# Optimization experiments

Measured on AMD Instinct MI355X. Metric: run time of the kernel, lower is better.

The kernel has to match this reference:

```python
import jax, jax.numpy as jnp
import numpy as np

B, H, W, C = 2, 128, 128, 96
L = H * W
NUM_HEADS = 6
D_STATE = 16
DT_RANK = 6  # ceil(96/16)
D_CONV = 4
MLP_HIDDEN = 4 * C


def _layernorm(x, g, b, eps=1e-5):
    m = x.mean(-1, keepdims=True)
    v = x.var(-1, keepdims=True)
    return (x - m) * jax.lax.rsqrt(v + eps) * g + b


def _dwconv2d(x, w, b):
    # x: [B,C,H,W], w: [C,1,3,3] depthwise, padding=1 (torch 'same' for k=3)
    y = jax.lax.conv_general_dilated(x, w, (1, 1), [(1, 1), (1, 1)],
                                     dimension_numbers=('NCHW', 'OIHW', 'NCHW'),
                                     feature_group_count=x.shape[1])
    return y + b[None, :, None, None]


def _dwconv1d(x, w):
    # x: [B,C,L], w: [C,1,4]; torch padding='same' for even k=4 pads (1,2); bias is None (conv_bias//2 == 0)
    return jax.lax.conv_general_dilated(x, w, (1,), [(1, 2)],
                                        dimension_numbers=('NCH', 'OIH', 'NCH'),
                                        feature_group_count=x.shape[1])


def _rope(x):
    # x: [b, H, W, c]; 2D axial rotary embedding, k_max = c//4 per axis
    b, h, w, c = x.shape
    k_max = c // 4
    theta = 1.0 / (10000.0 ** (jnp.arange(k_max, dtype=jnp.float32) / k_max))
    ang_h = jnp.broadcast_to(jnp.arange(h, dtype=jnp.float32)[:, None, None] * theta, (h, w, k_max))
    ang_w = jnp.broadcast_to(jnp.arange(w, dtype=jnp.float32)[None, :, None] * theta, (h, w, k_max))
    angles = jnp.concatenate([ang_h, ang_w], -1)  # [h,w,c//2]
    cos, sin = jnp.cos(angles), jnp.sin(angles)
    xr, xi = x[..., 0::2], x[..., 1::2]  # consecutive pairs -> complex
    out_r = xr * cos - xi * sin
    out_i = xr * sin + xi * cos
    return jnp.stack([out_r, out_i], -1).reshape(x.shape)


def _linear_attention(x, qk_w, qk_b, lepe_w, lepe_b):
    # x: [b, n, c]
    b, n, c = x.shape
    hd = c // NUM_HEADS
    qk = x @ qk_w + qk_b  # [b,n,2c]
    q = jax.nn.elu(qk[..., :c]) + 1.0
    k = jax.nn.elu(qk[..., c:]) + 1.0
    v = x
    q_r = _rope(q.reshape(b, H, W, c)).reshape(b, n, NUM_HEADS, hd).transpose(0, 2, 1, 3)
    k_r = _rope(k.reshape(b, H, W, c)).reshape(b, n, NUM_HEADS, hd).transpose(0, 2, 1, 3)
    qh = q.reshape(b, n, NUM_HEADS, hd).transpose(0, 2, 1, 3)
    kh = k.reshape(b, n, NUM_HEADS, hd).transpose(0, 2, 1, 3)
    vh = v.reshape(b, n, NUM_HEADS, hd).transpose(0, 2, 1, 3)
    kmean = kh.mean(axis=2, keepdims=True)  # [b,h,1,hd]
    zden = 1.0 / (jnp.einsum('bhnd,bhmd->bhnm', qh, kmean) + 1e-6)  # [b,h,n,1]
    scale = n ** (-0.5)
    kv = jnp.einsum('bhnd,bhne->bhde', k_r * scale, vh * scale)  # [b,h,hd,hd]
    out = jnp.einsum('bhnd,bhde->bhne', q_r, kv) * zden
    out = out.transpose(0, 2, 1, 3).reshape(b, n, c)
    v2d = v.reshape(b, H, W, c).transpose(0, 3, 1, 2)
    lepe = _dwconv2d(v2d, lepe_w, lepe_b).transpose(0, 2, 3, 1).reshape(b, n, c)
    return out + lepe


def _selective_scan(u, delta, A, Bm, Cm, Dv):
    # u, delta: [b,d,l]; A: [d,n]; Bm, Cm: [b,n,l]; Dv: [d]
    dA = jnp.exp(jnp.einsum('bdl,dn->lbdn', delta, A))
    dBu = jnp.einsum('bdl,bnl,bdl->lbdn', delta, Bm, u)
    Ct = jnp.moveaxis(Cm, -1, 0)  # [l,b,n]

    def step(hcar, inp):
        dA_t, dBu_t, C_t = inp
        hcar = dA_t * hcar + dBu_t  # [b,d,n]
        y_t = jnp.einsum('bdn,bn->bd', hcar, C_t)
        return hcar, y_t

    h0 = jnp.zeros(dA.shape[1:], dtype=u.dtype)
    _, ys = jax.lax.scan(step, h0, (dA, dBu, Ct))  # ys: [l,b,d]
    y = jnp.moveaxis(ys, 0, -1)  # [b,d,l]
    return y + Dv[None, :, None] * u


def setup_inputs() -> dict:
    key = jax.random.key(0)
    ks = iter(jax.random.split(key, 40))

    def rn(shape, s=0.02):
        return jax.random.normal(next(ks), shape, jnp.float32) * s

    dt = jnp.exp(jax.random.uniform(next(ks), (C,), jnp.float32)
                 * (np.log(0.1) - np.log(0.001)) + np.log(0.001))
    dt_proj_b = dt + jnp.log(-jnp.expm1(-dt))
    return {
        'hidden_states': jax.random.normal(next(ks), (B, L, C), jnp.float32),
        'norm_in_g': jnp.ones((C,), jnp.float32),
        'norm_in_b': jnp.zeros((C,), jnp.float32),
        'in_proj_w': rn((C, 3 * C)),
        'dw_w': rn((C, 1, 3, 3)),
        'dw_b': rn((C,)),
        'qk_w': rn((C, 2 * C)),
        'qk_b': rn((2 * C,)),
        'lepe_w': rn((C, 1, 3, 3)),
        'lepe_b': rn((C,)),
        'conv_x_w': rn((C, 1, D_CONV)),
        'conv_z_w': rn((C, 1, D_CONV)),
        'x_proj_w': rn((C, DT_RANK + 2 * D_STATE)),
        'dt_proj_w': rn((DT_RANK, C), DT_RANK ** -0.5),
        'dt_proj_b': dt_proj_b,
        'A_log': jnp.log(jnp.broadcast_to(jnp.arange(1, D_STATE + 1, dtype=jnp.float32), (C, D_STATE)) + 0.0),
        'D': jnp.ones((C,), jnp.float32),
        'out_proj_w': rn((2 * C, C)),
        'proj_out_w': rn((C, C)),
        'proj_out_b': rn((C,)),
        'out_w': rn((2 * C, C)),
        'out_b': rn((C,)),
        'norm_mlp_g': jnp.ones((C,), jnp.float32),
        'norm_mlp_b': jnp.zeros((C,), jnp.float32),
        'fc1_w': rn((C, MLP_HIDDEN)),
        'fc1_b': rn((MLP_HIDDEN,)),
        'fc2_w': rn((MLP_HIDDEN, C)),
        'fc2_b': rn((C,)),
    }


def reference(hidden_states, norm_in_g, norm_in_b, in_proj_w, dw_w, dw_b, qk_w, qk_b,
              lepe_w, lepe_b, conv_x_w, conv_z_w, x_proj_w, dt_proj_w, dt_proj_b,
              A_log, D, out_proj_w, proj_out_w, proj_out_b, out_w, out_b,
              norm_mlp_g, norm_mlp_b, fc1_w, fc1_b, fc2_w, fc2_b):
    b, l, c = hidden_states.shape
    shortcut = hidden_states
    hs = _layernorm(hidden_states, norm_in_g, norm_in_b)
    xzw = jnp.transpose(hs @ in_proj_w, (0, 2, 1))  # [b,3c,l]
    x, z, w_ = jnp.split(xzw, 3, axis=1)  # each [b,c,l]
    # linear-attention branch
    lin_x = jax.nn.silu(_dwconv2d(w_.reshape(b, c, H, W), dw_w, dw_b))
    lin_x = jnp.transpose(lin_x, (0, 2, 3, 1)).reshape(b, l, c)
    lin_x = _linear_attention(lin_x, qk_w, qk_b, lepe_w, lepe_b)
    # selective-scan branch
    A = -jnp.exp(A_log)
    x = jax.nn.silu(_dwconv1d(x, conv_x_w))
    z = jax.nn.silu(_dwconv1d(z, conv_z_w))
    x_dbl = jnp.einsum('bdl,de->ble', x, x_proj_w)
    dt = x_dbl[..., :DT_RANK]
    Bm = jnp.transpose(x_dbl[..., DT_RANK:DT_RANK + D_STATE], (0, 2, 1))
    Cm = jnp.transpose(x_dbl[..., DT_RANK + D_STATE:], (0, 2, 1))
    delta = jax.nn.softplus(jnp.einsum('blr,rd->bdl', dt, dt_proj_w) + dt_proj_b[None, :, None])
    y = _selective_scan(x, delta, A, Bm, Cm, D)
    y = jnp.concatenate([y, z], axis=1)  # [b,2c,l]
    out1 = jnp.transpose(y, (0, 2, 1)) @ out_proj_w  # [b,l,c]
    z_t = jnp.transpose(z, (0, 2, 1))
    out2 = (lin_x * z_t) @ proj_out_w + proj_out_b
    out = jnp.concatenate([out1, out2], -1) @ out_w + out_b
    out = shortcut + out
    h2 = _layernorm(out, norm_mlp_g, norm_mlp_b)
    h2 = jax.nn.gelu(h2 @ fc1_w + fc1_b, approximate=False)
    return out + (h2 @ fc2_w + fc2_b)
```

## Files before the change

### kernel.cpp

```cpp
#include <hip/hip_runtime.h>
#include <hip/hip_bf16.h>
#include <math.h>

#define B_ 2
#define H_ 128
#define W_ 128
#define C_ 96
#define L_ (H_*W_)
#define BL_ (B_*L_)
#define NH_ 6
#define NPROJ_ 38
#define MLPH_ 384
#define NCH_ 512
#define CHL_ (L_/NCH_)
#define NG_ 32

typedef __attribute__((ext_vector_type(8))) short bf16x8;
typedef __attribute__((ext_vector_type(4))) float f32x4;

#define MFMA16(a,b,c) __builtin_amdgcn_mfma_f32_16x16x32_bf16(a,b,c,0,0,0)

#define WOFF1 0
#define WOFF2 54
#define WOFF3 90
#define WOFF4 126
#define WOFF5 144
#define WOFF6 180
#define WOFF7 252
#define WOFF8 324
#define WFRAGS 333

__device__ __forceinline__ float siluf(float x){ return x / (1.f + __expf(-x)); }
__device__ __forceinline__ unsigned short f2bf(float x){
    __hip_bfloat16 h = __float2bfloat16(x);
    return *reinterpret_cast<unsigned short*>(&h);
}
__device__ __forceinline__ unsigned pack2(float a, float b){
    return (unsigned)f2bf(a) | ((unsigned)f2bf(b) << 16);
}
__device__ __forceinline__ float bf2f(unsigned short u){
    return __uint_as_float((unsigned)u << 16);
}
__device__ __forceinline__ float gelu_fast(float x){
    float u_ = 0.7978845608f*x*(1.f + 0.044715f*x*x);
    float au = fabsf(u_);
    float e = __expf(-2.f*au);
    float th = (1.f - e)/(1.f + e);
    th = copysignf(th, u_);
    return 0.5f*x*(1.f + th);
}

__global__ __launch_bounds__(64) void k_setup(const float* __restrict__ w1,
    const float* __restrict__ w2, const float* __restrict__ w3,
    const float* __restrict__ w4, const float* __restrict__ w5,
    const float* __restrict__ w6, const float* __restrict__ w7,
    const float* __restrict__ dww, const float* __restrict__ lw,
    const float* __restrict__ xpw, const float* __restrict__ cxw,
    const float* __restrict__ czw,
    unsigned short* __restrict__ dst, float2* __restrict__ ctab,
    float* __restrict__ wt9, float* __restrict__ lw9, float* __restrict__ kvacc,
    float* __restrict__ wxT, float* __restrict__ wzT)
{
    int m = blockIdx.y;
    int l = threadIdx.x;
    if (m < 7){
        const float* srcs[7] = {w1,w2,w3,w4,w5,w6,w7};
        const int Ks[7]   = {96,96,192,96,192,96,384};
        const int Ns[7]   = {288,192,96,96,96,384,96};
        const int offs[7] = {WOFF1,WOFF2,WOFF3,WOFF4,WOFF5,WOFF6,WOFF7};
        int f = blockIdx.x;
        int nnt = Ns[m] >> 4, nkf = Ks[m] >> 5;
        if (f >= nnt*nkf) return;
        int kf = f / nnt, nt = f - kf*nnt;
        const float* s = srcs[m];
        unsigned short* d = dst + ((size_t)(offs[m] + f)*64 + l)*8;
        int krow = kf*32 + (l>>4)*8;
        int col  = nt*16 + (l&15);
        #pragma unroll
        for (int j=0;j<8;j++) d[j] = f2bf(s[(size_t)(krow+j)*Ns[m] + col]);
    } else {
        int x = blockIdx.x;
        if (x == 0){
            for (int i=l; i<128*24; i+=64){
                int pos = i/24, p = i%24;
                float th = powf(10000.f, -(float)p/24.f);
                float sn, cs; sincosf((float)pos*th, &sn, &cs);
                ctab[i] = make_float2(cs, sn);
            }
        } else if (x == 1){
            for (int i=l; i<3264; i+=64) kvacc[i] = 0.f;
        } else if (x == 2){
            for (int i=l; i<864; i+=64){
                int c = i/9, tap = i%9;
                wt9[tap*96 + c] = dww[i];
                lw9[tap*96 + c] = lw[i];
            }
        } else if (x == 3){
            for (int f=0; f<9; f++){
                int kf=f/3, nt=f%3;
                unsigned short* d = dst + ((size_t)(WOFF8 + f)*64 + l)*8;
                int krow = kf*32 + (l>>4)*8;
                int col  = nt*16 + (l&15);
                #pragma unroll
                for (int j=0;j<8;j++){
                    float v = (col < NPROJ_) ? xpw[(size_t)(krow+j)*NPROJ_ + col] : 0.f;
                    d[j] = f2bf(v);
                }
            }
        } else if (x == 4){
            for (int i=l; i<384; i+=64){
                int j = i/96, c = i%96;
                wxT[i] = cxw[c*4 + j];
                wzT[i] = czw[c*4 + j];
            }
        }
    }
}

__global__ __launch_bounds__(256) void k_ln_inproj_m(const float* __restrict__ hs,
    const float* __restrict__ gg, const float* __restrict__ bb,
    const unsigned short* __restrict__ wbf,
    float* __restrict__ xx, float* __restrict__ zz, float* __restrict__ ww)
{
    __shared__ unsigned short A[64*128];
    int t = threadIdx.x;
    size_t row0 = (size_t)blockIdx.x * 64;
    {
        int r = t >> 2, q = t & 3;
        const float* src = hs + (row0 + r)*C_ + q*24;
        float v[24];
        float s=0.f, s2=0.f;
        #pragma unroll
        for (int i=0;i<24;i++){ float x=src[i]; v[i]=x; s+=x; s2+=x*x; }
        s += __shfl_xor(s,1); s2 += __shfl_xor(s2,1);
        s += __shfl_xor(s,2); s2 += __shfl_xor(s2,2);
        float mn = s*(1.f/C_);
        float rs = rsqrtf(s2*(1.f/C_) - mn*mn + 1e-5f);
        int base = r*128, sw = (r&7)<<3;
        #pragma unroll
        for (int i=0;i<24;i+=2){
            int c = q*24 + i;
            float a0 = (v[i]  -mn)*rs*gg[c]   + bb[c];
            float a1 = (v[i+1]-mn)*rs*gg[c+1] + bb[c+1];
            *(unsigned*)&A[base + (c ^ sw)] = pack2(a0,a1);
        }
    }
    __syncthreads();
    int w = t>>6, l = t&63, lr = l&15, lh = l>>4;
    int arow = w*16 + lr;
    int abase = arow*128, asw = (arow&7)<<3;
    bf16x8 af[3];
    #pragma unroll
    for (int kf=0;kf<3;kf++)
        af[kf] = *(const bf16x8*)&A[abase + ((kf*32 + lh*8) ^ asw)];
    #pragma unroll 2
    for (int nt=0; nt<18; nt++){
        f32x4 acc = {0.f,0.f,0.f,0.f};
        #pragma unroll
        for (int kf=0;kf<3;kf++){
            bf16x8 bf_ = *(const bf16x8*)(wbf + ((size_t)((WOFF1 + kf*18 + nt)*64 + l))*8);
            acc = MFMA16(af[kf], bf_, acc);
        }
        float* base_;
        if (nt < 6) base_ = xx; else if (nt < 12) base_ = zz; else base_ = ww;
        int col = (nt%6)*16 + lr;
        float* dst = base_ + (row0 + w*16 + lh*4)*C_ + col;
        #pragma unroll
        for (int j=0;j<4;j++) dst[(size_t)j*C_] = acc[j];
    }
}

__global__ __launch_bounds__(256) void k_dwconv2d(const float* __restrict__ wwb,
    const float* __restrict__ wt9, const float* __restrict__ dwb,
    float* __restrict__ out)
{
    int gid = blockIdx.x*256 + threadIdx.x;
    int row = gid/24, c4 = gid%24; int c = c4*4;
    int b = row >> 14;
    int ll = row & (L_-1);
    int h = ll >> 7, wq = ll & 127;
    float4 acc = {0.f,0.f,0.f,0.f};
    #pragma unroll
    for (int kh=0; kh<3; kh++){
        int hh = h + kh - 1;
        if ((unsigned)hh < 128u){
            int base_row = (b<<14) + (hh<<7);
            #pragma unroll
            for (int kw=0; kw<3; kw++){
                int wp = wq + kw - 1;
                if ((unsigned)wp < 128u){
                    float4 v = *(const float4*)&wwb[(size_t)(base_row + wp)*C_ + c];
                    float4 wt = *(const float4*)&wt9[(kh*3+kw)*96 + c];
                    acc.x += v.x*wt.x; acc.y += v.y*wt.y;
                    acc.z += v.z*wt.z; acc.w += v.w*wt.w;
                }
            }
        }
    }
    float4 bv = *(const float4*)&dwb[c];
    float4 o;
    o.x = siluf(acc.x+bv.x); o.y = siluf(acc.y+bv.y);
    o.z = siluf(acc.z+bv.z); o.w = siluf(acc.w+bv.w);
    *(float4*)&out[(size_t)row*C_ + c] = o;
}

__global__ __launch_bounds__(256) void k_conv1d_xdbl(const float* __restrict__ xxb,
    const float* __restrict__ zzb, const float* __restrict__ wxT,
    const float* __restrict__ wzT, const unsigned short* __restrict__ wbf,
    const float* __restrict__ dtw, const float* __restrict__ dtb,
    float* __restrict__ xs, float* __restrict__ zs,
    float* __restrict__ delta, float* __restrict__ BC)
{
    __shared__ unsigned short A[64*128];
    __shared__ float XD[64][8];
    __shared__ float dtws[6][96];
    int t = threadIdx.x;
    size_t row0 = (size_t)blockIdx.x * 64;
    int b = (int)(row0 >> 14);
    int l0 = (int)(row0 & 16383);
    for (int i=t; i<576; i+=256) dtws[i/96][i%96] = dtw[i];
    for (int p=t; p<64*24; p+=256){
        int r = p/24, cq = p - r*24, c = cq*4;
        int l = l0 + r;
        float ax0=0.f,ax1=0.f,ax2=0.f,ax3=0.f;
        float az0=0.f,az1=0.f,az2=0.f,az3=0.f;
        #pragma unroll
        for (int j=0;j<4;j++){
            int lq = l - 1 + j;
            if ((unsigned)lq < (unsigned)L_){
                size_t off = ((size_t)(b<<14) + lq)*C_ + c;
                float4 xv = *(const float4*)&xxb[off];
                float4 zv = *(const float4*)&zzb[off];
                float4 wx4 = *(const float4*)&wxT[j*96 + c];
                float4 wz4 = *(const float4*)&wzT[j*96 + c];
                ax0 += xv.x*wx4.x; ax1 += xv.y*wx4.y; ax2 += xv.z*wx4.z; ax3 += xv.w*wx4.w;
                az0 += zv.x*wz4.x; az1 += zv.y*wz4.y; az2 += zv.z*wz4.z; az3 += zv.w*wz4.w;
            }
        }
        ax0=siluf(ax0); ax1=siluf(ax1); ax2=siluf(ax2); ax3=siluf(ax3);
        az0=siluf(az0); az1=siluf(az1); az2=siluf(az2); az3=siluf(az3);
        float4 xo={ax0,ax1,ax2,ax3}, zo={az0,az1,az2,az3};
        *(float4*)&xs[(row0+r)*C_ + c] = xo;
        *(float4*)&zs[(row0+r)*C_ + c] = zo;
        int sw = (r&7)<<3;
        uint2 pk = { pack2(ax0,ax1), pack2(ax2,ax3) };
        *(uint2*)&A[r*128 + (c ^ sw)] = pk;
    }
    __syncthreads();
    int w=t>>6, l=t&63, lr=l&15, lh=l>>4;
    int arow = w*16+lr, asw=(arow&7)<<3;
    bf16x8 af[3];
    #pragma unroll
    for (int kf=0;kf<3;kf++)
        af[kf] = *(const bf16x8*)&A[arow*128 + ((kf*32 + lh*8) ^ asw)];
    #pragma unroll
    for (int nt=0; nt<3; nt++){
        f32x4 acc={0.f,0.f,0.f,0.f};
        #pragma unroll
        for (int kf=0;kf<3;kf++){
            bf16x8 bfr=*(const bf16x8*)(wbf + ((size_t)((WOFF8 + kf*3 + nt)*64 + l))*8);
            acc = MFMA16(af[kf], bfr, acc);
        }
        int col = nt*16 + lr;
        #pragma unroll
        for (int j=0;j<4;j++){
            int row = w*16 + lh*4 + j;
            if (col < 6) XD[row][col] = acc[j];
            else if (col < NPROJ_) BC[(row0+row)*32 + (col-6)] = acc[j];
        }
    }
    __syncthreads();
    {
        int r = t>>2, q = t&3;
        float xd0=XD[r][0], xd1=XD[r][1], xd2=XD[r][2];
        float xd3=XD[r][3], xd4=XD[r][4], xd5=XD[r][5];
        #pragma unroll
        for (int g=0; g<6; g++){
            int c = q*24 + g*4;
            float4 acc = *(const float4*)&dtb[c];
            float4 w0 = *(const float4*)&dtws[0][c];
            float4 w1 = *(const float4*)&dtws[1][c];
            float4 w2 = *(const float4*)&dtws[2][c];
            float4 w3 = *(const float4*)&dtws[3][c];
            float4 w4 = *(const float4*)&dtws[4][c];
            float4 w5 = *(const float4*)&dtws[5][c];
            acc.x += xd0*w0.x + xd1*w1.x + xd2*w2.x + xd3*w3.x + xd4*w4.x + xd5*w5.x;
            acc.y += xd0*w0.y + xd1*w1.y + xd2*w2.y + xd3*w3.y + xd4*w4.y + xd5*w5.y;
            acc.z += xd0*w0.z + xd1*w1.z + xd2*w2.z + xd3*w3.z + xd4*w4.z + xd5*w5.z;
            acc.w += xd0*w0.w + xd1*w1.w + xd2*w2.w + xd3*w3.w + xd4*w4.w + xd5*w5.w;
            float4 dl;
            dl.x = (acc.x>20.f)? acc.x : __logf(1.f+__expf(acc.x));
            dl.y = (acc.y>20.f)? acc.y : __logf(1.f+__expf(acc.y));
            dl.z = (acc.z>20.f)? acc.z : __logf(1.f+__expf(acc.z));
            dl.w = (acc.w>20.f)? acc.w : __logf(1.f+__expf(acc.w));
            *(float4*)&delta[(row0+r)*C_ + c] = dl;
        }
    }
}

__global__ __launch_bounds__(256) void k_qk_kv(const float* __restrict__ lin,
    const unsigned short* __restrict__ wbf, const float* __restrict__ qkb,
    const float2* __restrict__ ctab, float* __restrict__ qo,
    float* __restrict__ kvacc)
{
    __shared__ unsigned short A[64*128];
    __shared__ float KR[64*105];
    __shared__ float kmsum[96];
    int t = threadIdx.x;
    size_t row0 = (size_t)blockIdx.x * 64;
    int b = (int)(row0 >> 14);
    int l0 = (int)(row0 & 16383);
    for (int p = t; p < 64*48; p += 256){
        int r = p/48, c = (p - r*48)*2;
        float2 xy = *(const float2*)&lin[(row0 + r)*C_ + c];
        *(unsigned*)&A[r*128 + (c ^ ((r&7)<<3))] = pack2(xy.x, xy.y);
    }
    if (t < 96) kmsum[t] = 0.f;
    __syncthreads();
    int w=t>>6, l=t&63, lr=l&15, lh=l>>4;
    int arow = w*16+lr; int asw=(arow&7)<<3;
    bf16x8 af[3];
    #pragma unroll
    for (int kf=0;kf<3;kf++)
        af[kf] = *(const bf16x8*)&A[arow*128 + ((kf*32 + lh*8) ^ asw)];
    #pragma unroll 2
    for (int nt=0; nt<12; nt++){
        f32x4 acc={0.f,0.f,0.f,0.f};
        #pragma unroll
        for (int kf=0;kf<3;kf++){
            bf16x8 bfr=*(const bf16x8*)(wbf + ((size_t)((WOFF2 + kf*12 + nt)*64 + l))*8);
            acc = MFMA16(af[kf], bfr, acc);
        }
        int colg = nt*16 + lr;
        float bias = qkb[colg];
        float vv[4];
        #pragma unroll
        for (int j=0;j<4;j++){
            float v = acc[j] + bias;
            vv[j] = (v>0.f)? v+1.f : __expf(v);
        }
        if (nt < 6){
            float* dp = qo + (row0 + w*16 + lh*4)*C_ + colg;
            #pragma unroll
            for (int j=0;j<4;j++) dp[(size_t)j*C_] = vv[j];
        } else {
            int ck = colg - 96;
            atomicAdd(&kmsum[ck], vv[0]+vv[1]+vv[2]+vv[3]);
            float pv[4];
            #pragma unroll
            for (int j=0;j<4;j++) pv[j] = __shfl_xor(vv[j], 1);
            int p = ck >> 1;
            #pragma unroll
            for (int j=0;j<4;j++){
                int rl = l0 + w*16 + lh*4 + j;
                int hp = rl>>7, wp = rl&127;
                float2 cssn = (p<24)? ctab[hp*24+p] : ctab[wp*24+(p-24)];
                float kr = (ck&1)? (pv[j]*cssn.y + vv[j]*cssn.x)
                                 : (vv[j]*cssn.x - pv[j]*cssn.y);
                KR[(w*16+lh*4+j)*105 + ck] = kr;
            }
        }
    }
    __syncthreads();
    for (int h = w; h < 6; h += 4){
        f32x4 acc = {0.f,0.f,0.f,0.f};
        #pragma unroll
        for (int kk=0; kk<2; kk++){
            union { bf16x8 v; unsigned short u[8]; } afu, bfu;
            #pragma unroll
            for (int j=0;j<8;j++){
                int rr = kk*32 + lh*8 + j;
                afu.u[j] = f2bf(KR[rr*105 + h*16 + lr]);
                bfu.u[j] = A[rr*128 + ((h*16+lr) ^ ((rr&7)<<3))];
            }
            acc = MFMA16(afu.v, bfu.v, acc);
        }
        #pragma unroll
        for (int i=0;i<4;i++)
            atomicAdd(&kvacc[b*1536 + h*256 + (lh*4+i)*16 + lr], acc[i]);
    }
    if (t < 96) atomicAdd(&kvacc[3072 + b*96 + t], kmsum[t]);
}

__global__ __launch_bounds__(384) void k_attnout(const float* __restrict__ qbuf,
    const float* __restrict__ vbuf, const float* __restrict__ kvacc,
    const float2* __restrict__ ctab, const float* __restrict__ lw9,
    const float* __restrict__ lb, float* __restrict__ aout)
{
    __shared__ float kvs[1536];
    __shared__ float kms[96];
    int t = threadIdx.x;
    size_t row0 = (size_t)blockIdx.x * 16;
    int b = (int)(row0 >> 14);
    const float invL = 1.f/16384.f;
    for (int i=t; i<1536; i+=384) kvs[i] = kvacc[b*1536+i]*invL;
    if (t < 96) kms[t] = kvacc[3072+b*96+t]*invL;
    __syncthreads();
    int r = t/24, c4 = t%24;
    int c = c4*4;
    int lrow = (int)(row0 & 16383) + r;
    int hp = lrow>>7, wp = lrow&127;
    size_t row = row0 + r;
    float4 q4 = *(const float4*)&qbuf[row*C_ + c];
    int p0 = c>>1, p1 = p0+1;
    float2 cs0 = (p0<24)? ctab[hp*24+p0] : ctab[wp*24+(p0-24)];
    float2 cs1 = (p1<24)? ctab[hp*24+p1] : ctab[wp*24+(p1-24)];
    float4 qr;
    qr.x = q4.x*cs0.x - q4.y*cs0.y;
    qr.y = q4.x*cs0.y + q4.y*cs0.x;
    qr.z = q4.z*cs1.x - q4.w*cs1.y;
    qr.w = q4.z*cs1.y + q4.w*cs1.x;
    int h = c4>>2, j = c4&3;
    int dbase = j*4;
    float zp = q4.x*kms[h*16+dbase]   + q4.y*kms[h*16+dbase+1]
             + q4.z*kms[h*16+dbase+2] + q4.w*kms[h*16+dbase+3];
    zp += __shfl_xor(zp,1);
    zp += __shfl_xor(zp,2);
    float zd = 1.f/(zp + 1e-6f);
    float4 o = {0.f,0.f,0.f,0.f};
    #pragma unroll
    for (int g=0; g<4; g++){
        float4 qg;
        if (g==0) qg = qr;
        else {
            qg.x=__shfl_xor(qr.x,g); qg.y=__shfl_xor(qr.y,g);
            qg.z=__shfl_xor(qr.z,g); qg.w=__shfl_xor(qr.w,g);
        }
        int db = ((j^g)<<2);
        const float* kp = &kvs[h*256 + db*16 + j*4];
        #pragma unroll
        for (int i=0;i<4;i++){
            float qi = (i==0)?qg.x:(i==1)?qg.y:(i==2)?qg.z:qg.w;
            float4 kv4 = *(const float4*)&kp[i*16];
            o.x += qi*kv4.x; o.y += qi*kv4.y;
            o.z += qi*kv4.z; o.w += qi*kv4.w;
        }
    }
    float4 acc = *(const float4*)&lb[c];
    #pragma unroll
    for (int kh=0; kh<3; kh++){
        int hh = hp + kh - 1;
        if ((unsigned)hh < 128u){
            int base_row = (b<<14) + (hh<<7);
            #pragma unroll
            for (int kw=0; kw<3; kw++){
                int wq = wp + kw - 1;
                if ((unsigned)wq < 128u){
                    float4 v = *(const float4*)&vbuf[(size_t)(base_row + wq)*C_ + c];
                    float4 wt = *(const float4*)&lw9[(kh*3+kw)*96 + c];
                    acc.x += v.x*wt.x; acc.y += v.y*wt.y;
                    acc.z += v.z*wt.z; acc.w += v.w*wt.w;
                }
            }
        }
    }
    float4 res;
    res.x = o.x*zd + acc.x; res.y = o.y*zd + acc.y;
    res.z = o.z*zd + acc.z; res.w = o.w*zd + acc.w;
    *(float4*)&aout[row*C_ + c] = res;
}

__global__ __launch_bounds__(384) void k_scan1(const float* __restrict__ delta,
    const float* __restrict__ xs, const float* __restrict__ BC,
    const float* __restrict__ A_log, float* __restrict__ Ap, float* __restrict__ Be)
{
    int t = threadIdx.x; int nq = t&3, c = t>>2;
    int blk = blockIdx.x; int b = blk>>9, ch = blk&(NCH_-1);
    float4 a4 = *(const float4*)&A_log[c*16 + nq*4];
    float a0=-__expf(a4.x), a1=-__expf(a4.y), a2=-__expf(a4.z), a3=-__expf(a4.w);
    float ap0=1.f,ap1=1.f,ap2=1.f,ap3=1.f;
    float be0=0.f,be1=0.f,be2=0.f,be3=0.f;
    size_t base = ((size_t)b<<14) + ch*CHL_;
    for (int i=0;i<CHL_;i++){
        size_t row = base + i;
        float dl = delta[row*C_+c];
        float u  = xs[row*C_+c];
        float du = dl*u;
        float4 bc = *(const float4*)&BC[row*32 + nq*4];
        float e0=__expf(dl*a0), e1=__expf(dl*a1), e2=__expf(dl*a2), e3=__expf(dl*a3);
        ap0*=e0; be0=be0*e0+du*bc.x;
        ap1*=e1; be1=be1*e1+du*bc.y;
        ap2*=e2; be2=be2*e2+du*bc.z;
        ap3*=e3; be3=be3*e3+du*bc.w;
    }
    size_t o = (size_t)blk*1536 + c*16 + nq*4;
    float4 apv={ap0,ap1,ap2,ap3}, bev={be0,be1,be2,be3};
    *(float4*)&Ap[o] = apv;
    *(float4*)&Be[o] = bev;
}

__global__ __launch_bounds__(384) void k_scan2a(const float* __restrict__ Ap,
    const float* __restrict__ Be, float* __restrict__ GA, float* __restrict__ GB)
{
    int t = threadIdx.x; int blk = blockIdx.x;
    int b = blk>>5, g = blk&(NG_-1);
    int idx = (t>>2)*16 + (t&3)*4;
    float4 A = {1.f,1.f,1.f,1.f}, Bv = {0.f,0.f,0.f,0.f};
    for (int j=0;j<16;j++){
        size_t o = ((size_t)(b*NCH_ + g*16 + j))*1536 + idx;
        float4 a = *(const float4*)&Ap[o];
        float4 bb = *(const float4*)&Be[o];
        Bv.x=a.x*Bv.x+bb.x; Bv.y=a.y*Bv.y+bb.y; Bv.z=a.z*Bv.z+bb.z; Bv.w=a.w*Bv.w+bb.w;
        A.x*=a.x; A.y*=a.y; A.z*=a.z; A.w*=a.w;
    }
    size_t o = (size_t)blk*1536 + idx;
    *(float4*)&GA[o] = A;
    *(float4*)&GB[o] = Bv;
}

__global__ __launch_bounds__(256) void k_scan2b(const float* __restrict__ GA,
    const float* __restrict__ GB, float* __restrict__ Gin)
{
    int t = blockIdx.x*256 + threadIdx.x;
    int b = t/1536, m = t%1536;
    float h = 0.f;
    for (int g=0; g<NG_; g++){
        size_t o = ((size_t)(b*NG_+g))*1536 + m;
        Gin[o] = h;
        h = GA[o]*h + GB[o];
    }
}

__global__ __launch_bounds__(384) void k_scan2c(const float* __restrict__ Ap,
    const float* __restrict__ Be, const float* __restrict__ Gin,
    float* __restrict__ Hin)
{
    int t = threadIdx.x; int blk = blockIdx.x;
    int b = blk>>5, g = blk&(NG_-1);
    int idx = (t>>2)*16 + (t&3)*4;
    float4 h = *(const float4*)&Gin[(size_t)blk*1536 + idx];
    for (int j=0;j<16;j++){
        size_t o = ((size_t)(b*NCH_ + g*16 + j))*1536 + idx;
        *(float4*)&Hin[o] = h;
        float4 a = *(const float4*)&Ap[o];
        float4 bb = *(const float4*)&Be[o];
        h.x=a.x*h.x+bb.x; h.y=a.y*h.y+bb.y; h.z=a.z*h.z+bb.z; h.w=a.w*h.w+bb.w;
    }
}

__global__ __launch_bounds__(384) void k_scan3(const float* __restrict__ delta,
    const float* __restrict__ xs, const float* __restrict__ BC,
    const float* __restrict__ A_log, const float* __restrict__ Dv,
    const float* __restrict__ Hin, float* __restrict__ y)
{
    int t = threadIdx.x; int nq = t&3, c = t>>2;
    int blk = blockIdx.x; int b = blk>>9, ch = blk&(NCH_-1);
    float4 a4 = *(const float4*)&A_log[c*16 + nq*4];
    float a0=-__expf(a4.x), a1=-__expf(a4.y), a2=-__expf(a4.z), a3=-__expf(a4.w);
    float4 h = *(const float4*)&Hin[(size_t)blk*1536 + c*16 + nq*4];
    float Dc = Dv[c];
    size_t base = ((size_t)b<<14) + ch*CHL_;
    for (int i=0;i<CHL_;i++){
        size_t row = base + i;
        float dl = delta[row*C_+c];
        float u  = xs[row*C_+c];
        float du = dl*u;
        float4 bcB = *(const float4*)&BC[row*32 + nq*4];
        float4 bcC = *(const float4*)&BC[row*32 + 16 + nq*4];
        float e0=__expf(dl*a0), e1=__expf(dl*a1), e2=__expf(dl*a2), e3=__expf(dl*a3);
        h.x=h.x*e0+du*bcB.x; h.y=h.y*e1+du*bcB.y;
        h.z=h.z*e2+du*bcB.z; h.w=h.w*e3+du*bcB.w;
        float yv = h.x*bcC.x + h.y*bcC.y + h.z*bcC.z + h.w*bcC.w;
        yv += __shfl_xor(yv,1);
        yv += __shfl_xor(yv,2);
        if (nq == 0) y[row*C_+c] = yv + Dc*u;
    }
}

__global__ __launch_bounds__(512) void k_combine_mlp(const float* __restrict__ y,
    const float* __restrict__ zs, const float* __restrict__ aout,
    const unsigned short* __restrict__ wbf, const float* __restrict__ pob,
    const float* __restrict__ outb, const float* __restrict__ hs,
    const float* __restrict__ gg, const float* __restrict__ bb,
    const float* __restrict__ f1b, const float* __restrict__ f2b,
    float* __restrict__ outr)
{
    __shared__ __attribute__((aligned(16))) char POOL[65536];
    __shared__ float LNS[64][2], LNS2[64][2];
    unsigned short* Y  = (unsigned short*)POOL;
    unsigned short* AZ = (unsigned short*)(POOL + 24576);
    unsigned short* C2 = (unsigned short*)(POOL + 40960);
    unsigned short* AT = (unsigned short*)POOL;
    unsigned short* HID= (unsigned short*)(POOL + 16384);
    int t=threadIdx.x;
    size_t row0=(size_t)blockIdx.x*64;
    for (int p=t;p<64*48;p+=512){
        int r=p/48, c=(p-r*48)*2;
        size_t g=(row0+r)*C_+c;
        float2 yv=*(const float2*)&y[g];
        float2 zv=*(const float2*)&zs[g];
        float2 av=*(const float2*)&aout[g];
        int sw=(r&7)<<3;
        *(unsigned*)&Y[r*192 + (c^sw)] = pack2(yv.x,yv.y);
        *(unsigned*)&Y[r*192 + ((96+c)^sw)] = pack2(zv.x,zv.y);
        *(unsigned*)&AZ[r*128 + (c^sw)] = pack2(av.x*zv.x, av.y*zv.y);
    }
    __syncthreads();
    int w=t>>6, l=t&63, lr=l&15, lh=l>>4;
    int rt=w>>1, hf=w&1;
    int arow=rt*16+lr; int asw=(arow&7)<<3;
    bf16x8 af1[6], af2[3];
    #pragma unroll
    for (int kf=0;kf<6;kf++) af1[kf]=*(const bf16x8*)&Y[arow*192 + ((kf*32+lh*8)^asw)];
    #pragma unroll
    for (int kf=0;kf<3;kf++) af2[kf]=*(const bf16x8*)&AZ[arow*128 + ((kf*32+lh*8)^asw)];
    #pragma unroll
    for (int q=0;q<3;q++){
        int nt = hf*3 + q;
        f32x4 a1={0.f,0.f,0.f,0.f}, a2={0.f,0.f,0.f,0.f};
        #pragma unroll
        for (int kf=0;kf<6;kf++){
            bf16x8 b=*(const bf16x8*)(wbf+((size_t)((WOFF3+kf*6+nt)*64+l))*8);
            a1=MFMA16(af1[kf],b,a1);
        }
        #pragma unroll
        for (int kf=0;kf<3;kf++){
            bf16x8 b=*(const bf16x8*)(wbf+((size_t)((WOFF4+kf*6+nt)*64+l))*8);
            a2=MFMA16(af2[kf],b,a2);
        }
        int col=nt*16+lr;
        float pb=pob[col];
        #pragma unroll
        for (int j=0;j<4;j++){
            int row=rt*16+lh*4+j;
            int sw2=(row&7)<<3;
            C2[row*192 + (col^sw2)] = f2bf(a1[j]);
            C2[row*192 + ((96+col)^sw2)] = f2bf(a2[j]+pb);
        }
    }
    __syncthreads();
    bf16x8 af3[6];
    #pragma unroll
    for (int kf=0;kf<6;kf++) af3[kf]=*(const bf16x8*)&C2[arow*192 + ((kf*32+lh*8)^asw)];
    float outv[3][4];
    #pragma unroll
    for (int q=0;q<3;q++){
        int nt = hf*3 + q;
        f32x4 acc={0.f,0.f,0.f,0.f};
        #pragma unroll
        for (int kf=0;kf<6;kf++){
            bf16x8 b=*(const bf16x8*)(wbf+((size_t)((WOFF5+kf*6+nt)*64+l))*8);
            acc=MFMA16(af3[kf],b,acc);
        }
        int col=nt*16+lr;
        float ob=outb[col];
        #pragma unroll
        for (int j=0;j<4;j++){
            size_t row=row0+rt*16+lh*4+j;
            outv[q][j] = acc[j] + ob + hs[row*C_+col];
        }
    }
    float s_[4], s2_[4];
    #pragma unroll
    for (int j=0;j<4;j++){
        float s=0.f, s2=0.f;
        #pragma unroll
        for (int q=0;q<3;q++){ float v=outv[q][j]; s+=v; s2+=v*v; }
        s_[j]=s; s2_[j]=s2;
    }
    #pragma unroll
    for (int m=1;m<16;m<<=1){
        #pragma unroll
        for (int j=0;j<4;j++){
            s_[j]  += __shfl_xor(s_[j],  m);
            s2_[j] += __shfl_xor(s2_[j], m);
        }
    }
    if (lr==0){
        #pragma unroll
        for (int j=0;j<4;j++){
            int row = rt*16+lh*4+j;
            LNS[row][hf]  = s_[j];
            LNS2[row][hf] = s2_[j];
        }
    }
    __syncthreads();
    #pragma unroll
    for (int j=0;j<4;j++){
        int row = rt*16+lh*4+j;
        float s  = LNS[row][0]  + LNS[row][1];
        float s2 = LNS2[row][0] + LNS2[row][1];
        float mn = s*(1.f/C_);
        float rs = rsqrtf(s2*(1.f/C_) - mn*mn + 1e-5f);
        int sw2 = (row&7)<<3;
        #pragma unroll
        for (int q=0;q<3;q++){
            int col = (hf*3+q)*16+lr;
            AT[row*128 + (col^sw2)] = f2bf((outv[q][j]-mn)*rs*gg[col]+bb[col]);
        }
    }
    __syncthreads();
    {
        bf16x8 af[3];
        #pragma unroll
        for(int kf=0;kf<3;kf++) af[kf]=*(const bf16x8*)&AT[arow*128+((kf*32+lh*8)^asw)];
        #pragma unroll 2
        for(int q=0;q<12;q++){
            int nt = hf*12 + q;
            f32x4 acc={0.f,0.f,0.f,0.f};
            #pragma unroll
            for(int kf=0;kf<3;kf++){
                bf16x8 b=*(const bf16x8*)(wbf+((size_t)((WOFF6+kf*24+nt)*64+l))*8);
                acc=MFMA16(af[kf],b,acc);
            }
            int col=nt*16+lr;
            float bias=f1b[col];
            #pragma unroll
            for(int j=0;j<4;j++){
                int row=rt*16+lh*4+j;
                HID[row*384 + (col^((row&7)<<3))] = f2bf(gelu_fast(acc[j]+bias));
            }
        }
    }
    __syncthreads();
    {
        bf16x8 afh[12];
        #pragma unroll
        for(int kf=0;kf<12;kf++) afh[kf]=*(const bf16x8*)&HID[arow*384+((kf*32+lh*8)^asw)];
        #pragma unroll
        for(int q=0;q<3;q++){
            int nt = hf*3 + q;
            f32x4 acc={0.f,0.f,0.f,0.f};
            #pragma unroll
            for(int kf=0;kf<12;kf++){
                bf16x8 b=*(const bf16x8*)(wbf+((size_t)((WOFF7+kf*6+nt)*64+l))*8);
                acc=MFMA16(afh[kf],b,acc);
            }
            int col=nt*16+lr;
            float bias=f2b[col];
            #pragma unroll
            for(int j=0;j<4;j++){
                size_t row=row0+rt*16+lh*4+j;
                outr[row*C_+col] = outv[q][j] + acc[j] + bias;
            }
        }
    }
}

extern "C" void kernel_launch(void* const* d_in, const int* in_sizes, int n_in,
                              void* d_out, int out_size, void* d_ws, size_t ws_size,
                              hipStream_t stream)
{
    const float* hs        = (const float*)d_in[0];
    const float* norm_in_g = (const float*)d_in[1];
    const float* norm_in_b = (const float*)d_in[2];
    const float* in_proj_w = (const float*)d_in[3];
    const float* dw_w      = (const float*)d_in[4];
    const float* dw_b      = (const float*)d_in[5];
    const float* qk_w      = (const float*)d_in[6];
    const float* qk_b      = (const float*)d_in[7];
    const float* lepe_w    = (const float*)d_in[8];
    const float* lepe_b    = (const float*)d_in[9];
    const float* conv_x_w  = (const float*)d_in[10];
    const float* conv_z_w  = (const float*)d_in[11];
    const float* x_proj_w  = (const float*)d_in[12];
    const float* dt_proj_w = (const float*)d_in[13];
    const float* dt_proj_b = (const float*)d_in[14];
    const float* A_log     = (const float*)d_in[15];
    const float* Dv        = (const float*)d_in[16];
    const float* out_proj_w= (const float*)d_in[17];
    const float* proj_out_w= (const float*)d_in[18];
    const float* proj_out_b= (const float*)d_in[19];
    const float* out_w     = (const float*)d_in[20];
    const float* out_b     = (const float*)d_in[21];
    const float* norm_mlp_g= (const float*)d_in[22];
    const float* norm_mlp_b= (const float*)d_in[23];
    const float* fc1_w     = (const float*)d_in[24];
    const float* fc1_b     = (const float*)d_in[25];
    const float* fc2_w     = (const float*)d_in[26];
    const float* fc2_b     = (const float*)d_in[27];

    float* ws = (float*)d_ws;
    size_t o = 0;
    float* xx    = ws + o; o += (size_t)BL_*C_;
    float* zz    = ws + o; o += (size_t)BL_*C_;
    float* wwb   = ws + o; o += (size_t)BL_*C_;
    float* lin_x = ws + o; o += (size_t)BL_*C_;
    float* xs    = ws + o; o += (size_t)BL_*C_;
    float* zs    = ws + o; o += (size_t)BL_*C_;
    float* delta = ws + o; o += (size_t)BL_*C_;
    float* BC    = ws + o; o += (size_t)BL_*32;
    float* Ap    = ws + o; o += (size_t)B_*NCH_*1536;
    float* Be    = ws + o; o += (size_t)B_*NCH_*1536;
    float* Hin   = ws + o; o += (size_t)B_*NCH_*1536;
    float* GA    = ws + o; o += (size_t)B_*NG_*1536;
    float* GB    = ws + o; o += (size_t)B_*NG_*1536;
    float* Gin   = ws + o; o += (size_t)B_*NG_*1536;
    float* kvacc = ws + o; o += 3264;
    float2* ctab = (float2*)(ws + o); o += 6144;
    float* wt9   = ws + o; o += 864;
    float* lw9   = ws + o; o += 864;
    float* wxT   = ws + o; o += 384;
    float* wzT   = ws + o; o += 384;
    unsigned short* wbf = (unsigned short*)(ws + o);

    float* qbuf = xx;
    float* ybuf = zz;
    float* aout = wwb;
    float* outr = (float*)d_out;

    k_setup<<<dim3(72,8), 64, 0, stream>>>(in_proj_w, qk_w, out_proj_w, proj_out_w,
                                           out_w, fc1_w, fc2_w, dw_w, lepe_w,
                                           x_proj_w, conv_x_w, conv_z_w,
                                           wbf, ctab, wt9, lw9, kvacc, wxT, wzT);
    k_ln_inproj_m<<<BL_/64, 256, 0, stream>>>(hs, norm_in_g, norm_in_b, wbf, xx, zz, wwb);
    k_dwconv2d<<<(BL_*24)/256, 256, 0, stream>>>(wwb, wt9, dw_b, lin_x);
    k_conv1d_xdbl<<<BL_/64, 256, 0, stream>>>(xx, zz, wxT, wzT, wbf,
                                              dt_proj_w, dt_proj_b, xs, zs, delta, BC);
    k_qk_kv<<<BL_/64, 256, 0, stream>>>(lin_x, wbf, qk_b, ctab, qbuf, kvacc);
    k_attnout<<<BL_/16, 384, 0, stream>>>(qbuf, lin_x, kvacc, ctab, lw9, lepe_b, aout);
    k_scan1<<<B_*NCH_, 384, 0, stream>>>(delta, xs, BC, A_log, Ap, Be);
    k_scan2a<<<B_*NG_, 384, 0, stream>>>(Ap, Be, GA, GB);
    k_scan2b<<<12, 256, 0, stream>>>(GA, GB, Gin);
    k_scan2c<<<B_*NG_, 384, 0, stream>>>(Ap, Be, Gin, Hin);
    k_scan3<<<B_*NCH_, 384, 0, stream>>>(delta, xs, BC, A_log, Dv, Hin, ybuf);
    k_combine_mlp<<<BL_/64, 512, 0, stream>>>(ybuf, zs, aout, wbf, proj_out_b,
                                              out_b, hs, norm_mlp_g, norm_mlp_b,
                                              fc1_b, fc2_b, outr);
}
```

Measured before the change: 203.2 us.

## Store intermediate activations as bf16 and fuse z gating into attention output

Intermediate buffers (in-projection x/z/w outputs, dwconv output, q, z-silu, scan y, gated attention output) are now written and read as bf16 instead of fp32. This roughly halves global memory traffic between the chain of kernels. The multiplication of the attention output by z moves into k_attnout, so k_combine_mlp loads MFMA A-fragments straight from global memory without the LDS staging pass. The cost is extra rounding of intermediates to bf16, which may hurt accuracy.

```diff
diff --git a/kernel.cpp b/kernel.cpp
--- a/kernel.cpp
+++ b/kernel.cpp
@@ -17,6 +17,7 @@
 
 typedef __attribute__((ext_vector_type(8))) short bf16x8;
 typedef __attribute__((ext_vector_type(4))) float f32x4;
+typedef __attribute__((ext_vector_type(4))) unsigned short us4v;
 
 #define MFMA16(a,b,c) __builtin_amdgcn_mfma_f32_16x16x32_bf16(a,b,c,0,0,0)
 
@@ -120,7 +121,8 @@
 __global__ __launch_bounds__(256) void k_ln_inproj_m(const float* __restrict__ hs,
     const float* __restrict__ gg, const float* __restrict__ bb,
     const unsigned short* __restrict__ wbf,
-    float* __restrict__ xx, float* __restrict__ zz, float* __restrict__ ww)
+    unsigned short* __restrict__ xx, unsigned short* __restrict__ zz,
+    unsigned short* __restrict__ ww)
 {
     __shared__ unsigned short A[64*128];
     int t = threadIdx.x;
@@ -161,25 +163,25 @@
             bf16x8 bf_ = *(const bf16x8*)(wbf + ((size_t)((WOFF1 + kf*18 + nt)*64 + l))*8);
             acc = MFMA16(af[kf], bf_, acc);
         }
-        float* base_;
+        unsigned short* base_;
         if (nt < 6) base_ = xx; else if (nt < 12) base_ = zz; else base_ = ww;
         int col = (nt%6)*16 + lr;
-        float* dst = base_ + (row0 + w*16 + lh*4)*C_ + col;
-        #pragma unroll
-        for (int j=0;j<4;j++) dst[(size_t)j*C_] = acc[j];
-    }
-}
-
-__global__ __launch_bounds__(256) void k_dwconv2d(const float* __restrict__ wwb,
+        unsigned short* dst = base_ + (row0 + w*16 + lh*4)*C_ + col;
+        #pragma unroll
+        for (int j=0;j<4;j++) dst[(size_t)j*C_] = f2bf(acc[j]);
+    }
+}
+
+__global__ __launch_bounds__(256) void k_dwconv2d(const unsigned short* __restrict__ wwb,
     const float* __restrict__ wt9, const float* __restrict__ dwb,
-    float* __restrict__ out)
+    unsigned short* __restrict__ out)
 {
     int gid = blockIdx.x*256 + threadIdx.x;
     int row = gid/24, c4 = gid%24; int c = c4*4;
     int b = row >> 14;
     int ll = row & (L_-1);
     int h = ll >> 7, wq = ll & 127;
-    float4 acc = {0.f,0.f,0.f,0.f};
+    float a0=0.f,a1=0.f,a2=0.f,a3=0.f;
     #pragma unroll
     for (int kh=0; kh<3; kh++){
         int hh = h + kh - 1;
@@ -189,26 +191,26 @@
             for (int kw=0; kw<3; kw++){
                 int wp = wq + kw - 1;
                 if ((unsigned)wp < 128u){
-                    float4 v = *(const float4*)&wwb[(size_t)(base_row + wp)*C_ + c];
+                    us4v v = *(const us4v*)&wwb[(size_t)(base_row + wp)*C_ + c];
                     float4 wt = *(const float4*)&wt9[(kh*3+kw)*96 + c];
-                    acc.x += v.x*wt.x; acc.y += v.y*wt.y;
-                    acc.z += v.z*wt.z; acc.w += v.w*wt.w;
+                    a0 += bf2f(v[0])*wt.x; a1 += bf2f(v[1])*wt.y;
+                    a2 += bf2f(v[2])*wt.z; a3 += bf2f(v[3])*wt.w;
                 }
             }
         }
     }
     float4 bv = *(const float4*)&dwb[c];
-    float4 o;
-    o.x = siluf(acc.x+bv.x); o.y = siluf(acc.y+bv.y);
-    o.z = siluf(acc.z+bv.z); o.w = siluf(acc.w+bv.w);
-    *(float4*)&out[(size_t)row*C_ + c] = o;
-}
-
-__global__ __launch_bounds__(256) void k_conv1d_xdbl(const float* __restrict__ xxb,
-    const float* __restrict__ zzb, const float* __restrict__ wxT,
+    us4v o;
+    o[0]=f2bf(siluf(a0+bv.x)); o[1]=f2bf(siluf(a1+bv.y));
+    o[2]=f2bf(siluf(a2+bv.z)); o[3]=f2bf(siluf(a3+bv.w));
+    *(us4v*)&out[(size_t)row*C_ + c] = o;
+}
+
+__global__ __launch_bounds__(256) void k_conv1d_xdbl(const unsigned short* __restrict__ xxb,
+    const unsigned short* __restrict__ zzb, const float* __restrict__ wxT,
     const float* __restrict__ wzT, const unsigned short* __restrict__ wbf,
     const float* __restrict__ dtw, const float* __restrict__ dtb,
-    float* __restrict__ xs, float* __restrict__ zs,
+    float* __restrict__ xs, unsigned short* __restrict__ zb,
     float* __restrict__ delta, float* __restrict__ BC)
 {
     __shared__ unsigned short A[64*128];
@@ -229,19 +231,22 @@
             int lq = l - 1 + j;
             if ((unsigned)lq < (unsigned)L_){
                 size_t off = ((size_t)(b<<14) + lq)*C_ + c;
-                float4 xv = *(const float4*)&xxb[off];
-                float4 zv = *(const float4*)&zzb[off];
+                us4v xv = *(const us4v*)&xxb[off];
+                us4v zv = *(const us4v*)&zzb[off];
                 float4 wx4 = *(const float4*)&wxT[j*96 + c];
                 float4 wz4 = *(const float4*)&wzT[j*96 + c];
-                ax0 += xv.x*wx4.x; ax1 += xv.y*wx4.y; ax2 += xv.z*wx4.z; ax3 += xv.w*wx4.w;
-                az0 += zv.x*wz4.x; az1 += zv.y*wz4.y; az2 += zv.z*wz4.z; az3 += zv.w*wz4.w;
+                ax0 += bf2f(xv[0])*wx4.x; ax1 += bf2f(xv[1])*wx4.y;
+                ax2 += bf2f(xv[2])*wx4.z; ax3 += bf2f(xv[3])*wx4.w;
+                az0 += bf2f(zv[0])*wz4.x; az1 += bf2f(zv[1])*wz4.y;
+                az2 += bf2f(zv[2])*wz4.z; az3 += bf2f(zv[3])*wz4.w;
             }
         }
         ax0=siluf(ax0); ax1=siluf(ax1); ax2=siluf(ax2); ax3=siluf(ax3);
         az0=siluf(az0); az1=siluf(az1); az2=siluf(az2); az3=siluf(az3);
-        float4 xo={ax0,ax1,ax2,ax3}, zo={az0,az1,az2,az3};
+        float4 xo={ax0,ax1,ax2,ax3};
         *(float4*)&xs[(row0+r)*C_ + c] = xo;
-        *(float4*)&zs[(row0+r)*C_ + c] = zo;
+        us4v zo; zo[0]=f2bf(az0); zo[1]=f2bf(az1); zo[2]=f2bf(az2); zo[3]=f2bf(az3);
+        *(us4v*)&zb[(row0+r)*C_ + c] = zo;
         int sw = (r&7)<<3;
         uint2 pk = { pack2(ax0,ax1), pack2(ax2,ax3) };
         *(uint2*)&A[r*128 + (c ^ sw)] = pk;
@@ -298,9 +303,9 @@
     }
 }
 
-__global__ __launch_bounds__(256) void k_qk_kv(const float* __restrict__ lin,
+__global__ __launch_bounds__(256) void k_qk_kv(const unsigned short* __restrict__ lin,
     const unsigned short* __restrict__ wbf, const float* __restrict__ qkb,
-    const float2* __restrict__ ctab, float* __restrict__ qo,
+    const float2* __restrict__ ctab, unsigned short* __restrict__ qo,
     float* __restrict__ kvacc)
 {
     __shared__ unsigned short A[64*128];
@@ -310,10 +315,10 @@
     size_t row0 = (size_t)blockIdx.x * 64;
     int b = (int)(row0 >> 14);
     int l0 = (int)(row0 & 16383);
-    for (int p = t; p < 64*48; p += 256){
-        int r = p/48, c = (p - r*48)*2;
-        float2 xy = *(const float2*)&lin[(row0 + r)*C_ + c];
-        *(unsigned*)&A[r*128 + (c ^ ((r&7)<<3))] = pack2(xy.x, xy.y);
+    for (int p = t; p < 64*12; p += 256){
+        int r = p/12, c = (p - r*12)*8;
+        int sw = (r&7)<<3;
+        *(uint4*)&A[r*128 + (c ^ sw)] = *(const uint4*)&lin[(row0+r)*C_ + c];
     }
     if (t < 96) kmsum[t] = 0.f;
     __syncthreads();
@@ -340,9 +345,9 @@
             vv[j] = (v>0.f)? v+1.f : __expf(v);
         }
         if (nt < 6){
-            float* dp = qo + (row0 + w*16 + lh*4)*C_ + colg;
-            #pragma unroll
-            for (int j=0;j<4;j++) dp[(size_t)j*C_] = vv[j];
+            unsigned short* dp = qo + (row0 + w*16 + lh*4)*C_ + colg;
+            #pragma unroll
+            for (int j=0;j<4;j++) dp[(size_t)j*C_] = f2bf(vv[j]);
         } else {
             int ck = colg - 96;
             atomicAdd(&kmsum[ck], vv[0]+vv[1]+vv[2]+vv[3]);
@@ -382,10 +387,11 @@
     if (t < 96) atomicAdd(&kvacc[3072 + b*96 + t], kmsum[t]);
 }
 
-__global__ __launch_bounds__(384) void k_attnout(const float* __restrict__ qbuf,
-    const float* __restrict__ vbuf, const float* __restrict__ kvacc,
-    const float2* __restrict__ ctab, const float* __restrict__ lw9,
-    const float* __restrict__ lb, float* __restrict__ aout)
+__global__ __launch_bounds__(384) void k_attnout(const unsigned short* __restrict__ qb,
+    const unsigned short* __restrict__ vb, const unsigned short* __restrict__ zb,
+    const float* __restrict__ kvacc, const float2* __restrict__ ctab,
+    const float* __restrict__ lw9, const float* __restrict__ lb,
+    unsigned short* __restrict__ azb)
 {
     __shared__ float kvs[1536];
     __shared__ float kms[96];
@@ -401,19 +407,20 @@
     int lrow = (int)(row0 & 16383) + r;
     int hp = lrow>>7, wp = lrow&127;
     size_t row = row0 + r;
-    float4 q4 = *(const float4*)&qbuf[row*C_ + c];
+    us4v qu = *(const us4v*)&qb[row*C_ + c];
+    float q0=bf2f(qu[0]), q1=bf2f(qu[1]), q2=bf2f(qu[2]), q3=bf2f(qu[3]);
     int p0 = c>>1, p1 = p0+1;
     float2 cs0 = (p0<24)? ctab[hp*24+p0] : ctab[wp*24+(p0-24)];
     float2 cs1 = (p1<24)? ctab[hp*24+p1] : ctab[wp*24+(p1-24)];
     float4 qr;
-    qr.x = q4.x*cs0.x - q4.y*cs0.y;
-    qr.y = q4.x*cs0.y + q4.y*cs0.x;
-    qr.z = q4.z*cs1.x - q4.w*cs1.y;
-    qr.w = q4.z*cs1.y + q4.w*cs1.x;
+    qr.x = q0*cs0.x - q1*cs0.y;
+    qr.y = q0*cs0.y + q1*cs0.x;
+    qr.z = q2*cs1.x - q3*cs1.y;
+    qr.w = q2*cs1.y + q3*cs1.x;
     int h = c4>>2, j = c4&3;
     int dbase = j*4;
-    float zp = q4.x*kms[h*16+dbase]   + q4.y*kms[h*16+dbase+1]
-             + q4.z*kms[h*16+dbase+2] + q4.w*kms[h*16+dbase+3];
+    float zp = q0*kms[h*16+dbase]   + q1*kms[h*16+dbase+1]
+             + q2*kms[h*16+dbase+2] + q3*kms[h*16+dbase+3];
     zp += __shfl_xor(zp,1);
     zp += __shfl_xor(zp,2);
     float zd = 1.f/(zp + 1e-6f);
@@ -446,18 +453,21 @@
             for (int kw=0; kw<3; kw++){
                 int wq = wp + kw - 1;
                 if ((unsigned)wq < 128u){
-                    float4 v = *(const float4*)&vbuf[(size_t)(base_row + wq)*C_ + c];
+                    us4v v = *(const us4v*)&vb[(size_t)(base_row + wq)*C_ + c];
                     float4 wt = *(const float4*)&lw9[(kh*3+kw)*96 + c];
-                    acc.x += v.x*wt.x; acc.y += v.y*wt.y;
-                    acc.z += v.z*wt.z; acc.w += v.w*wt.w;
+                    acc.x += bf2f(v[0])*wt.x; acc.y += bf2f(v[1])*wt.y;
+                    acc.z += bf2f(v[2])*wt.z; acc.w += bf2f(v[3])*wt.w;
                 }
             }
         }
     }
-    float4 res;
-    res.x = o.x*zd + acc.x; res.y = o.y*zd + acc.y;
-    res.z = o.z*zd + acc.z; res.w = o.w*zd + acc.w;
-    *(float4*)&aout[row*C_ + c] = res;
+    us4v zu = *(const us4v*)&zb[row*C_ + c];
+    us4v res;
+    res[0] = f2bf((o.x*zd + acc.x)*bf2f(zu[0]));
+    res[1] = f2bf((o.y*zd + acc.y)*bf2f(zu[1]));
+    res[2] = f2bf((o.z*zd + acc.z)*bf2f(zu[2]));
+    res[3] = f2bf((o.w*zd + acc.w)*bf2f(zu[3]));
+    *(us4v*)&azb[row*C_ + c] = res;
 }
 
 __global__ __launch_bounds__(384) void k_scan1(const float* __restrict__ delta,
@@ -541,7 +551,7 @@
 __global__ __launch_bounds__(384) void k_scan3(const float* __restrict__ delta,
     const float* __restrict__ xs, const float* __restrict__ BC,
     const float* __restrict__ A_log, const float* __restrict__ Dv,
-    const float* __restrict__ Hin, float* __restrict__ y)
+    const float* __restrict__ Hin, unsigned short* __restrict__ y)
 {
     int t = threadIdx.x; int nq = t&3, c = t>>2;
     int blk = blockIdx.x; int b = blk>>9, ch = blk&(NCH_-1);
@@ -563,12 +573,12 @@
         float yv = h.x*bcC.x + h.y*bcC.y + h.z*bcC.z + h.w*bcC.w;
         yv += __shfl_xor(yv,1);
         yv += __shfl_xor(yv,2);
-        if (nq == 0) y[row*C_+c] = yv + Dc*u;
-    }
-}
-
-__global__ __launch_bounds__(512) void k_combine_mlp(const float* __restrict__ y,
-    const float* __restrict__ zs, const float* __restrict__ aout,
+        if (nq == 0) y[row*C_+c] = f2bf(yv + Dc*u);
+    }
+}
+
+__global__ __launch_bounds__(512) void k_combine_mlp(const unsigned short* __restrict__ yb,
+    const unsigned short* __restrict__ zb, const unsigned short* __restrict__ azb,
     const unsigned short* __restrict__ wbf, const float* __restrict__ pob,
     const float* __restrict__ outb, const float* __restrict__ hs,
     const float* __restrict__ gg, const float* __restrict__ bb,
@@ -577,33 +587,22 @@
 {
     __shared__ __attribute__((aligned(16))) char POOL[65536];
     __shared__ float LNS[64][2], LNS2[64][2];
-    unsigned short* Y  = (unsigned short*)POOL;
-    unsigned short* AZ = (unsigned short*)(POOL + 24576);
-    unsigned short* C2 = (unsigned short*)(POOL + 40960);
+    unsigned short* C2 = (unsigned short*)POOL;
     unsigned short* AT = (unsigned short*)POOL;
     unsigned short* HID= (unsigned short*)(POOL + 16384);
     int t=threadIdx.x;
     size_t row0=(size_t)blockIdx.x*64;
-    for (int p=t;p<64*48;p+=512){
-        int r=p/48, c=(p-r*48)*2;
-        size_t g=(row0+r)*C_+c;
-        float2 yv=*(const float2*)&y[g];
-        float2 zv=*(const float2*)&zs[g];
-        float2 av=*(const float2*)&aout[g];
-        int sw=(r&7)<<3;
-        *(unsigned*)&Y[r*192 + (c^sw)] = pack2(yv.x,yv.y);
-        *(unsigned*)&Y[r*192 + ((96+c)^sw)] = pack2(zv.x,zv.y);
-        *(unsigned*)&AZ[r*128 + (c^sw)] = pack2(av.x*zv.x, av.y*zv.y);
-    }
-    __syncthreads();
     int w=t>>6, l=t&63, lr=l&15, lh=l>>4;
     int rt=w>>1, hf=w&1;
     int arow=rt*16+lr; int asw=(arow&7)<<3;
+    size_t gbase = (row0+arow)*C_;
     bf16x8 af1[6], af2[3];
     #pragma unroll
-    for (int kf=0;kf<6;kf++) af1[kf]=*(const bf16x8*)&Y[arow*192 + ((kf*32+lh*8)^asw)];
-    #pragma unroll
-    for (int kf=0;kf<3;kf++) af2[kf]=*(const bf16x8*)&AZ[arow*128 + ((kf*32+lh*8)^asw)];
+    for (int kf=0;kf<3;kf++){
+        af1[kf]   = *(const bf16x8*)&yb[gbase + kf*32 + lh*8];
+        af1[3+kf] = *(const bf16x8*)&zb[gbase + kf*32 + lh*8];
+        af2[kf]   = *(const bf16x8*)&azb[gbase + kf*32 + lh*8];
+    }
     #pragma unroll
     for (int q=0;q<3;q++){
         int nt = hf*3 + q;
@@ -772,12 +771,13 @@
 
     float* ws = (float*)d_ws;
     size_t o = 0;
-    float* xx    = ws + o; o += (size_t)BL_*C_;
-    float* zz    = ws + o; o += (size_t)BL_*C_;
-    float* wwb   = ws + o; o += (size_t)BL_*C_;
-    float* lin_x = ws + o; o += (size_t)BL_*C_;
+    const size_t USH = (size_t)BL_*C_/2;
+    unsigned short* xxb  = (unsigned short*)(ws + o); o += USH;
+    unsigned short* zzb  = (unsigned short*)(ws + o); o += USH;
+    unsigned short* wwb  = (unsigned short*)(ws + o); o += USH;
+    unsigned short* linb = (unsigned short*)(ws + o); o += USH;
+    unsigned short* zbuf = (unsigned short*)(ws + o); o += USH;
     float* xs    = ws + o; o += (size_t)BL_*C_;
-    float* zs    = ws + o; o += (size_t)BL_*C_;
     float* delta = ws + o; o += (size_t)BL_*C_;
     float* BC    = ws + o; o += (size_t)BL_*32;
     float* Ap    = ws + o; o += (size_t)B_*NCH_*1536;
@@ -794,27 +794,28 @@
     float* wzT   = ws + o; o += 384;
     unsigned short* wbf = (unsigned short*)(ws + o);
 
-    float* qbuf = xx;
-    float* ybuf = zz;
-    float* aout = wwb;
+    unsigned short* qb  = xxb;
+    unsigned short* yb  = zzb;
+    unsigned short* azb = wwb;
     float* outr = (float*)d_out;
 
     k_setup<<<dim3(72,8), 64, 0, stream>>>(in_proj_w, qk_w, out_proj_w, proj_out_w,
                                            out_w, fc1_w, fc2_w, dw_w, lepe_w,
                                            x_proj_w, conv_x_w, conv_z_w,
                                            wbf, ctab, wt9, lw9, kvacc, wxT, wzT);
-    k_ln_inproj_m<<<BL_/64, 256, 0, stream>>>(hs, norm_in_g, norm_in_b, wbf, xx, zz, wwb);
-    k_dwconv2d<<<(BL_*24)/256, 256, 0, stream>>>(wwb, wt9, dw_b, lin_x);
-    k_conv1d_xdbl<<<BL_/64, 256, 0, stream>>>(xx, zz, wxT, wzT, wbf,
-                                              dt_proj_w, dt_proj_b, xs, zs, delta, BC);
-    k_qk_kv<<<BL_/64, 256, 0, stream>>>(lin_x, wbf, qk_b, ctab, qbuf, kvacc);
-    k_attnout<<<BL_/16, 384, 0, stream>>>(qbuf, lin_x, kvacc, ctab, lw9, lepe_b, aout);
+    k_ln_inproj_m<<<BL_/64, 256, 0, stream>>>(hs, norm_in_g, norm_in_b, wbf,
+                                              xxb, zzb, wwb);
+    k_dwconv2d<<<(BL_*24)/256, 256, 0, stream>>>(wwb, wt9, dw_b, linb);
+    k_conv1d_xdbl<<<BL_/64, 256, 0, stream>>>(xxb, zzb, wxT, wzT, wbf,
+                                              dt_proj_w, dt_proj_b, xs, zbuf, delta, BC);
+    k_qk_kv<<<BL_/64, 256, 0, stream>>>(linb, wbf, qk_b, ctab, qb, kvacc);
+    k_attnout<<<BL_/16, 384, 0, stream>>>(qb, linb, zbuf, kvacc, ctab, lw9, lepe_b, azb);
     k_scan1<<<B_*NCH_, 384, 0, stream>>>(delta, xs, BC, A_log, Ap, Be);
     k_scan2a<<<B_*NG_, 384, 0, stream>>>(Ap, Be, GA, GB);
     k_scan2b<<<12, 256, 0, stream>>>(GA, GB, Gin);
     k_scan2c<<<B_*NG_, 384, 0, stream>>>(Ap, Be, Gin, Hin);
-    k_scan3<<<B_*NCH_, 384, 0, stream>>>(delta, xs, BC, A_log, Dv, Hin, ybuf);
-    k_combine_mlp<<<BL_/64, 512, 0, stream>>>(ybuf, zs, aout, wbf, proj_out_b,
+    k_scan3<<<B_*NCH_, 384, 0, stream>>>(delta, xs, BC, A_log, Dv, Hin, yb);
+    k_combine_mlp<<<BL_/64, 512, 0, stream>>>(yb, zbuf, azb, wbf, proj_out_b,
                                               out_b, hs, norm_mlp_g, norm_mlp_b,
                                               fc1_b, fc2_b, outr);
 }
```

Result: faster. 191.8 us (-5.6%).
